# Kernel optimization log

Measured on AMD Instinct MI355X. Metric: run time of the kernel, lower is better.

Reference implementation:

```python
import jax, jax.numpy as jnp
import numpy as np
import math

EPS_NORM = 1e-6
EPS_COS = 1e-6


def _rms_norm(x, scale, eps):
    ms = jnp.mean(jnp.square(x), axis=-1, keepdims=True)
    return x * (scale * jax.lax.rsqrt(ms + eps))


def _apply_rope(x, theta):
    # x: [n, nh, s, e], theta: [n, nh, s, d] with 2*d <= e
    d = theta.shape[-1]
    x1, x2, rest = x[..., :d], x[..., d:2 * d], x[..., 2 * d:]
    cos, sin = jnp.cos(theta), jnp.sin(theta)
    y1 = x1 * cos - x2 * sin
    y2 = x2 * cos + x1 * sin
    return jnp.concatenate([y1, y2, rest], axis=-1)


def _make_freqs(d_head, n_heads):
    dim = d_head // 2
    log_min, log_max = math.log(math.pi), math.log(10.0 * math.pi)
    f = np.exp(np.linspace(log_min, log_max, n_heads * dim // 4 + 1, dtype=np.float64)[:-1])
    return jnp.asarray(f.reshape(dim // 4, n_heads).T, dtype=jnp.float32)  # [n_heads, dim//4]


def setup_inputs() -> dict:
    key = jax.random.key(0)
    ks = jax.random.split(key, 8)
    n, H, W, d_model = 4, 32, 32, 1024
    d_head, n_heads, cond_f = 64, 16, 1024
    x = jax.random.normal(ks[0], (n, H, W, d_model), dtype=jnp.float32)
    pos = jax.random.uniform(ks[1], (n, H, W, 2), dtype=jnp.float32) * 2.0 - 1.0
    cond = jax.random.normal(ks[2], (n, cond_f), dtype=jnp.float32)
    norm_scale = jnp.ones((d_model,), dtype=jnp.float32)
    ada_w = jax.random.normal(ks[3], (3 * d_model, cond_f), dtype=jnp.float32) * 0.02
    ada_b = jnp.zeros((3 * d_model,), dtype=jnp.float32)
    qkv_w = jax.random.normal(ks[4], (3 * d_model, d_model), dtype=jnp.float32) * 0.02
    attn_scale = jnp.full((n_heads,), 10.0, dtype=jnp.float32)
    out_w = jax.random.normal(ks[5], (d_model, d_model), dtype=jnp.float32) * 0.02
    freqs = _make_freqs(d_head, n_heads)
    return {"x": x, "pos": pos, "cond": cond, "norm_scale": norm_scale,
            "ada_w": ada_w, "ada_b": ada_b, "qkv_w": qkv_w,
            "attn_scale": attn_scale, "out_w": out_w, "freqs": freqs}


def reference(x, pos, cond, norm_scale, ada_w, ada_b, qkv_w, attn_scale, out_w, freqs):
    n, H, W, d_model = x.shape
    n_heads, nf = freqs.shape          # nf = d_head//4... actually (d_head//2)//4
    d_head = d_model // n_heads
    s = H * W
    skip = x
    # adaLN modulation
    mod = jax.nn.silu(cond) @ ada_w.T + ada_b              # [n, 3*d_model]
    shift, scale, gate = jnp.split(mod, 3, axis=-1)        # each [n, d_model]
    xn = _rms_norm(x, norm_scale, EPS_NORM)
    xm = xn * (1.0 + scale[:, None, None, :]) + shift[:, None, None, :]
    # qkv projection: layout (t nh e) on last dim
    qkv = (xm @ qkv_w.T).reshape(n, s, 3, n_heads, d_head)
    q, k, v = qkv[:, :, 0], qkv[:, :, 1], qkv[:, :, 2]     # [n, s, nh, e]
    q = jnp.transpose(q, (0, 2, 1, 3))                     # [n, nh, s, e]
    k = jnp.transpose(k, (0, 2, 1, 3))
    v = jnp.transpose(v, (0, 2, 1, 3))
    # cosine-sim scaling per head
    sqrt_scale = jnp.sqrt(attn_scale)[None, :, None, None]
    q = q * (sqrt_scale * jax.lax.rsqrt(jnp.sum(jnp.square(q), axis=-1, keepdims=True) + EPS_COS))
    k = k * (sqrt_scale * jax.lax.rsqrt(jnp.sum(jnp.square(k), axis=-1, keepdims=True) + EPS_COS))
    # axial RoPE angles
    posf = pos.reshape(n, s, 2)
    theta_h = posf[:, :, None, 0:1] * freqs                # [n, s, nh, nf]
    theta_w = posf[:, :, None, 1:2] * freqs
    theta = jnp.concatenate([theta_h, theta_w], axis=-1)   # [n, s, nh, 2*nf]
    theta = jnp.transpose(theta, (0, 2, 1, 3))             # [n, nh, s, 2*nf]
    q = _apply_rope(q, theta)
    k = _apply_rope(k, theta)
    # attention with softmax scale 1.0 (cosine-sim already scaled)
    scores = jnp.einsum('bnse,bnte->bnst', q, k)
    attn = jax.nn.softmax(scores, axis=-1)
    o = jnp.einsum('bnst,bnte->bnse', attn, v)             # [n, nh, s, e]
    o = jnp.transpose(o, (0, 2, 1, 3)).reshape(n, H, W, d_model)
    o = o @ out_w.T
    return skip + gate[:, None, None, :] * o
```

## Files before the change

### kernel.cpp

```cpp
#include <hip/hip_runtime.h>
#include <stdint.h>

typedef __bf16 bf16x8 __attribute__((ext_vector_type(8)));
typedef uint16_t u16x8 __attribute__((ext_vector_type(8)));
typedef uint16_t u16x4 __attribute__((ext_vector_type(4)));
typedef float f32x4 __attribute__((ext_vector_type(4)));

#define DEV static __device__ __forceinline__

DEV uint16_t f2bf(float f) {
  union { float f; uint32_t u; } v; v.f = f;
  return (uint16_t)((v.u + 0x8000u) >> 16);
}
DEV float bf2f(uint16_t h) {
  union { uint32_t u; float f; } v; v.u = ((uint32_t)h) << 16;
  return v.f;
}

#define GLOAD_LDS16(g, l)                                                     \
  __builtin_amdgcn_global_load_lds(                                           \
      (__attribute__((address_space(1))) void*)(g),                           \
      (__attribute__((address_space(3))) void*)(l), 16, 0, 0)

DEV void conv4(const float* __restrict__ src, uint16_t* __restrict__ dst, int n4,
               int tid, int nth) {
  const float4* s4 = (const float4*)src;
  for (int i = tid; i < n4; i += nth) {
    float4 v = s4[i];
    u16x4 o;
    o[0] = f2bf(v.x); o[1] = f2bf(v.y); o[2] = f2bf(v.z); o[3] = f2bf(v.w);
    *reinterpret_cast<u16x4*>(dst + (size_t)i * 4) = o;
  }
}

__global__ __launch_bounds__(256) void k_prep(
    const float* __restrict__ qkv_w, uint16_t* __restrict__ qkvw_bf,
    const float* __restrict__ out_w, uint16_t* __restrict__ outw_bf,
    const float* __restrict__ cond, const float* __restrict__ ada_w,
    const float* __restrict__ ada_b, float* __restrict__ mod) {
  int blk = blockIdx.x, t = threadIdx.x;
  if (blk < 3072) {
    int w = t >> 6, lane = t & 63;
    int gid = blk * 4 + w;
    int b = gid / 3072, j = gid - b * 3072;
    const float* cw = cond + b * 1024;
    const float* aw = ada_w + (size_t)j * 1024;
    float sum = 0.f;
    for (int i = 0; i < 16; ++i) {
      int f = lane + (i << 6);
      float c = cw[f];
      sum += (c / (1.f + __expf(-c))) * aw[f];
    }
    for (int m = 32; m; m >>= 1) sum += __shfl_xor(sum, m, 64);
    if (lane == 0) mod[b * 3072 + j] = sum + ada_b[j];
  } else if (blk < 3072 + 768) {
    conv4(qkv_w, qkvw_bf, 786432, (blk - 3072) * 256 + t, 768 * 256);
  } else {
    conv4(out_w, outw_bf, 262144, (blk - 3840) * 256 + t, 256 * 256);
  }
}

__global__ void k_norm_mod(const float* __restrict__ x, const float* __restrict__ norm_scale,
                           const float* __restrict__ mod, uint16_t* __restrict__ xm) {
  int row = blockIdx.x;
  int b = row >> 10;
  const float* xr = x + (size_t)row * 1024;
  const float* shiftp = mod + b * 3072;
  const float* scalep = shiftp + 1024;
  int t = threadIdx.x;
  float v[4];
  float s = 0.f;
  for (int i = 0; i < 4; ++i) { v[i] = xr[t + (i << 8)]; s += v[i] * v[i]; }
  for (int m = 32; m; m >>= 1) s += __shfl_xor(s, m, 64);
  __shared__ float red[4];
  if ((t & 63) == 0) red[t >> 6] = s;
  __syncthreads();
  s = red[0] + red[1] + red[2] + red[3];
  float inv = rsqrtf(s * (1.f / 1024.f) + 1e-6f);
  uint16_t* xo = xm + (size_t)row * 1024;
  for (int i = 0; i < 4; ++i) {
    int c = t + (i << 8);
    float val = v[i] * inv * norm_scale[c];
    val = val * (1.f + scalep[c]) + shiftp[c];
    xo[c] = f2bf(val);
  }
}

template <int N, int EPI>
__global__ __launch_bounds__(256) void k_gemm(const uint16_t* __restrict__ A,
                                              const uint16_t* __restrict__ B,
                                              uint16_t* __restrict__ Cbf,
                                              const float* __restrict__ skip,
                                              const float* __restrict__ modp,
                                              float* __restrict__ Cout) {
  constexpr int K = 1024;
  __shared__ uint16_t As[128 * 32];
  __shared__ uint16_t Bs[128 * 32];
  int t = threadIdx.x;
  int lane = t & 63;
  int w = t >> 6, wr = w >> 1, wc = w & 1;
  int bm = blockIdx.y, bn = blockIdx.x;
  f32x4 acc[4][4] = {};
  const size_t a_base = (size_t)(bm * 128) * K;
  const size_t b_base = (size_t)(bn * 128) * K;
  int r = t >> 2, cch = t & 3;
  for (int kt = 0; kt < K / 32; ++kt) {
    __syncthreads();
#pragma unroll
    for (int i = 0; i < 2; ++i) {
      int rr = r + (i << 6);
      int cs = (cch ^ ((rr >> 1) & 3)) << 3;
      GLOAD_LDS16(A + a_base + (size_t)rr * K + kt * 32 + cs, As + rr * 32 + (cch << 3));
      GLOAD_LDS16(B + b_base + (size_t)rr * K + kt * 32 + cs, Bs + rr * 32 + (cch << 3));
    }
    __syncthreads();
    bf16x8 af[4], bfr[4];
    int lq = lane >> 4;
#pragma unroll
    for (int m = 0; m < 4; ++m) {
      int R = wr * 64 + m * 16 + (lane & 15);
      af[m] = *reinterpret_cast<const bf16x8*>(&As[R * 32 + ((lq ^ ((R >> 1) & 3)) << 3)]);
    }
#pragma unroll
    for (int n = 0; n < 4; ++n) {
      int R = wc * 64 + n * 16 + (lane & 15);
      bfr[n] = *reinterpret_cast<const bf16x8*>(&Bs[R * 32 + ((lq ^ ((R >> 1) & 3)) << 3)]);
    }
#pragma unroll
    for (int m = 0; m < 4; ++m)
#pragma unroll
      for (int n = 0; n < 4; ++n)
        acc[m][n] = __builtin_amdgcn_mfma_f32_16x16x32_bf16(af[m], bfr[n], acc[m][n], 0, 0, 0);
  }
  int row0 = bm * 128 + wr * 64;
  int col0 = bn * 128 + wc * 64;
#pragma unroll
  for (int m = 0; m < 4; ++m)
#pragma unroll
    for (int n = 0; n < 4; ++n)
#pragma unroll
      for (int rr = 0; rr < 4; ++rr) {
        int R = row0 + m * 16 + ((lane >> 4) << 2) + rr;
        int C = col0 + n * 16 + (lane & 15);
        float v = acc[m][n][rr];
        if (EPI == 0) {
          Cbf[(size_t)R * N + C] = f2bf(v);
        } else {
          float g = modp[(R >> 10) * 3072 + 2048 + C];
          Cout[(size_t)R * N + C] = skip[(size_t)R * N + C] + g * v;
        }
      }
}

__global__ __launch_bounds__(256) void k_qkvpost(
    const uint16_t* __restrict__ qkv, const float* __restrict__ pos,
    const float* __restrict__ freqs, const float* __restrict__ attn_scale,
    uint16_t* __restrict__ Qb, uint16_t* __restrict__ Kb, uint16_t* __restrict__ Vt) {
  __shared__ uint16_t vtile[64 * 66];
  int t = threadIdx.x;
  int st = blockIdx.x, bh = blockIdx.y;
  int b = bh >> 4, h = bh & 15;
  int r = t >> 2;
  int s = t & 3;
  int sp = st * 64 + r;
  size_t m = (size_t)b * 1024 + sp;
  const uint16_t* basep = qkv + m * 3072 + h * 64 + s * 16;
  bf16x8 q0 = *reinterpret_cast<const bf16x8*>(basep);
  bf16x8 q1 = *reinterpret_cast<const bf16x8*>(basep + 8);
  bf16x8 k0 = *reinterpret_cast<const bf16x8*>(basep + 1024);
  bf16x8 k1 = *reinterpret_cast<const bf16x8*>(basep + 1032);
  u16x8 v0 = *reinterpret_cast<const u16x8*>(basep + 2048);
  u16x8 v1 = *reinterpret_cast<const u16x8*>(basep + 2056);
  float qv[16], kv[16];
#pragma unroll
  for (int i = 0; i < 8; ++i) {
    qv[i] = (float)q0[i]; qv[8 + i] = (float)q1[i];
    kv[i] = (float)k0[i]; kv[8 + i] = (float)k1[i];
  }
  float sq = 0.f, sk = 0.f;
#pragma unroll
  for (int i = 0; i < 16; ++i) { sq += qv[i] * qv[i]; sk += kv[i] * kv[i]; }
  sq += __shfl_xor(sq, 1, 64); sq += __shfl_xor(sq, 2, 64);
  sk += __shfl_xor(sk, 1, 64); sk += __shfl_xor(sk, 2, 64);
  float ss = sqrtf(attn_scale[h]);
  float qs = ss * rsqrtf(sq + 1e-6f);
  float ks = ss * rsqrtf(sk + 1e-6f);
#pragma unroll
  for (int i = 0; i < 16; ++i) { qv[i] *= qs; kv[i] *= ks; }
  float p0 = pos[m * 2], p1 = pos[m * 2 + 1];
  float sgn = (s == 0) ? -1.f : 1.f;
#pragma unroll
  for (int i = 0; i < 16; ++i) {
    float pq = __shfl_xor(qv[i], 1, 64);
    float pk = __shfl_xor(kv[i], 1, 64);
    if (s < 2) {
      float th = ((i < 8) ? p0 : p1) * freqs[h * 8 + (i & 7)];
      float sn, cs;
      __sincosf(th, &sn, &cs);
      qv[i] = qv[i] * cs + sgn * pq * sn;
      kv[i] = kv[i] * cs + sgn * pk * sn;
    }
  }
  bf16x8 qo0, qo1, ko0, ko1;
#pragma unroll
  for (int i = 0; i < 8; ++i) {
    qo0[i] = (__bf16)qv[i]; qo1[i] = (__bf16)qv[8 + i];
    ko0[i] = (__bf16)kv[i]; ko1[i] = (__bf16)kv[8 + i];
  }
  size_t qkb = ((size_t)bh * 1024 + sp) * 64 + s * 16;
  *reinterpret_cast<bf16x8*>(Qb + qkb) = qo0;
  *reinterpret_cast<bf16x8*>(Qb + qkb + 8) = qo1;
  *reinterpret_cast<bf16x8*>(Kb + qkb) = ko0;
  *reinterpret_cast<bf16x8*>(Kb + qkb + 8) = ko1;
#pragma unroll
  for (int i = 0; i < 8; ++i) {
    vtile[(s * 16 + i) * 66 + r] = v0[i];
    vtile[(s * 16 + 8 + i) * 66 + r] = v1[i];
  }
  __syncthreads();
  int d = t >> 2, c = t & 3;
  u16x8 w0, w1;
#pragma unroll
  for (int i = 0; i < 8; ++i) {
    w0[i] = vtile[d * 66 + c * 16 + i];
    w1[i] = vtile[d * 66 + c * 16 + 8 + i];
  }
  size_t vb = ((size_t)bh * 64 + d) * 1024 + st * 64 + c * 16;
  *reinterpret_cast<u16x8*>(Vt + vb) = w0;
  *reinterpret_cast<u16x8*>(Vt + vb + 8) = w1;
}

__global__ __launch_bounds__(512) void k_attn(const uint16_t* __restrict__ Qb,
                                              const uint16_t* __restrict__ Kb,
                                              const uint16_t* __restrict__ Vt,
                                              uint16_t* __restrict__ obuf) {
  __shared__ uint16_t Ks[64 * 64];
  __shared__ uint16_t Vs[64 * 64];
  __shared__ uint16_t Ps[8][16 * 88];
  int t = threadIdx.x, lane = t & 63, w = t >> 6;
  int qt = blockIdx.y, bh = blockIdx.x;
  int b = bh >> 4, h = bh & 15;
  int qrow = qt * 128 + w * 16 + (lane & 15);
  int klo = (lane >> 4) << 3;
  const uint16_t* qptr = Qb + ((size_t)bh * 1024 + qrow) * 64 + klo;
  bf16x8 qf0 = *reinterpret_cast<const bf16x8*>(qptr);
  bf16x8 qf1 = *reinterpret_cast<const bf16x8*>(qptr + 32);
  f32x4 oacc[4] = {};
  float denom[4] = {0.f, 0.f, 0.f, 0.f};
  const size_t kbase = (size_t)bh * 1024 * 64;
  const size_t vbase = (size_t)bh * 64 * 1024;
  for (int kt = 0; kt < 16; ++kt) {
    __syncthreads();
    {
      int row = t >> 3;
      int ce = ((t & 7) ^ (row & 7)) << 3;
      GLOAD_LDS16(Kb + kbase + (size_t)(kt * 64 + row) * 64 + ce, Ks + t * 8);
      GLOAD_LDS16(Vt + vbase + (size_t)row * 1024 + kt * 64 + ce, Vs + t * 8);
    }
    __syncthreads();
    bf16x8 pa0, pa1;
    {
      f32x4 s[4];
      for (int n = 0; n < 4; ++n) {
        int row = n * 16 + (lane & 15);
        int sw = (row & 7) << 3;
        bf16x8 kf0 = *reinterpret_cast<const bf16x8*>(&Ks[row * 64 + (klo ^ sw)]);
        bf16x8 kf1 = *reinterpret_cast<const bf16x8*>(&Ks[row * 64 + ((32 + klo) ^ sw)]);
        f32x4 z = {};
        z = __builtin_amdgcn_mfma_f32_16x16x32_bf16(qf0, kf0, z, 0, 0, 0);
        z = __builtin_amdgcn_mfma_f32_16x16x32_bf16(qf1, kf1, z, 0, 0, 0);
        s[n] = z;
      }
      for (int n = 0; n < 4; ++n)
        for (int rr = 0; rr < 4; ++rr) {
          float p = __expf(s[n][rr]);
          denom[rr] += p;
          Ps[w][(((lane >> 4) << 2) + rr) * 88 + n * 16 + (lane & 15)] = f2bf(p);
        }
      pa0 = *reinterpret_cast<const bf16x8*>(&Ps[w][(lane & 15) * 88 + klo]);
      pa1 = *reinterpret_cast<const bf16x8*>(&Ps[w][(lane & 15) * 88 + 32 + klo]);
    }
    for (int dt = 0; dt < 4; ++dt) {
      int row = dt * 16 + (lane & 15);
      int sw = (row & 7) << 3;
      bf16x8 vf0 = *reinterpret_cast<const bf16x8*>(&Vs[row * 64 + (klo ^ sw)]);
      bf16x8 vf1 = *reinterpret_cast<const bf16x8*>(&Vs[row * 64 + ((32 + klo) ^ sw)]);
      oacc[dt] = __builtin_amdgcn_mfma_f32_16x16x32_bf16(pa0, vf0, oacc[dt], 0, 0, 0);
      oacc[dt] = __builtin_amdgcn_mfma_f32_16x16x32_bf16(pa1, vf1, oacc[dt], 0, 0, 0);
    }
  }
  for (int rr = 0; rr < 4; ++rr)
    for (int msk = 8; msk; msk >>= 1) denom[rr] += __shfl_xor(denom[rr], msk, 64);
  for (int rr = 0; rr < 4; ++rr) {
    float rinv = 1.f / denom[rr];
    int sp = qt * 128 + w * 16 + ((lane >> 4) << 2) + rr;
    size_t orow = ((size_t)b * 1024 + sp) * 1024 + h * 64;
    for (int dt = 0; dt < 4; ++dt)
      obuf[orow + dt * 16 + (lane & 15)] = f2bf(oacc[dt][rr] * rinv);
  }
}

extern "C" void kernel_launch(void* const* d_in, const int* in_sizes, int n_in,
                              void* d_out, int out_size, void* d_ws, size_t ws_size,
                              hipStream_t stream) {
  const float* x = (const float*)d_in[0];
  const float* pos = (const float*)d_in[1];
  const float* cond = (const float*)d_in[2];
  const float* norm_scale = (const float*)d_in[3];
  const float* ada_w = (const float*)d_in[4];
  const float* ada_b = (const float*)d_in[5];
  const float* qkv_w = (const float*)d_in[6];
  const float* attn_scale = (const float*)d_in[7];
  const float* out_w = (const float*)d_in[8];
  const float* freqs = (const float*)d_in[9];
  float* out = (float*)d_out;
  char* ws = (char*)d_ws;
  float* mod = (float*)(ws + 0);
  uint16_t* xm = (uint16_t*)(ws + 65536);
  uint16_t* qkvw_bf = (uint16_t*)(ws + 8454144);
  uint16_t* outw_bf = (uint16_t*)(ws + 14745600);
  uint16_t* qkv = (uint16_t*)(ws + 16842752);
  uint16_t* Qb = (uint16_t*)(ws + 42008576);
  uint16_t* Kb = (uint16_t*)(ws + 50397184);
  uint16_t* Vt = (uint16_t*)(ws + 58785792);
  uint16_t* obuf = (uint16_t*)(ws + 67174400);

  k_prep<<<dim3(4096), dim3(256), 0, stream>>>(qkv_w, qkvw_bf, out_w, outw_bf,
                                               cond, ada_w, ada_b, mod);
  k_norm_mod<<<dim3(4096), dim3(256), 0, stream>>>(x, norm_scale, mod, xm);
  k_gemm<3072, 0><<<dim3(24, 32), dim3(256), 0, stream>>>(xm, qkvw_bf, qkv, nullptr, nullptr, nullptr);
  k_qkvpost<<<dim3(16, 64), dim3(256), 0, stream>>>(qkv, pos, freqs, attn_scale, Qb, Kb, Vt);
  k_attn<<<dim3(64, 8), dim3(512), 0, stream>>>(Qb, Kb, Vt, obuf);
  k_gemm<1024, 1><<<dim3(8, 32), dim3(256), 0, stream>>>(obuf, outw_bf, nullptr, x, mod, out);
}
```

Baseline: 118.2 us.

## Vectorize norm kernel, shrink out-proj GEMM tile, fold log2e into Q scaling

The RMS-norm/modulation kernel now reads float4 vectors and writes four bf16 values per thread instead of strided scalar accesses. The output projection GEMM gets its own kernel with 128x64 tiles, launching 512 blocks instead of 256 so more CUs are busy on the 1024-wide output. The log2(e) factor is folded into the Q scale so attention can use exp2f in place of __expf. The smaller tile lowers data reuse per block, and the exp2 rewrite is only mathematically equivalent up to rounding.

```diff
diff --git a/kernel.cpp b/kernel.cpp
--- a/kernel.cpp
+++ b/kernel.cpp
@@ -11,10 +11,6 @@
 DEV uint16_t f2bf(float f) {
   union { float f; uint32_t u; } v; v.f = f;
   return (uint16_t)((v.u + 0x8000u) >> 16);
-}
-DEV float bf2f(uint16_t h) {
-  union { uint32_t u; float f; } v; v.u = ((uint32_t)h) << 16;
-  return v.f;
 }
 
 #define GLOAD_LDS16(g, l)                                                     \
@@ -64,36 +60,33 @@
                            const float* __restrict__ mod, uint16_t* __restrict__ xm) {
   int row = blockIdx.x;
   int b = row >> 10;
-  const float* xr = x + (size_t)row * 1024;
-  const float* shiftp = mod + b * 3072;
-  const float* scalep = shiftp + 1024;
   int t = threadIdx.x;
-  float v[4];
-  float s = 0.f;
-  for (int i = 0; i < 4; ++i) { v[i] = xr[t + (i << 8)]; s += v[i] * v[i]; }
+  const float4* xr4 = (const float4*)(x + (size_t)row * 1024);
+  const float4* ns4 = (const float4*)norm_scale;
+  const float4* sh4 = (const float4*)(mod + b * 3072);
+  const float4* sc4 = (const float4*)(mod + b * 3072 + 1024);
+  float4 v = xr4[t];
+  float s = v.x * v.x + v.y * v.y + v.z * v.z + v.w * v.w;
   for (int m = 32; m; m >>= 1) s += __shfl_xor(s, m, 64);
   __shared__ float red[4];
   if ((t & 63) == 0) red[t >> 6] = s;
   __syncthreads();
   s = red[0] + red[1] + red[2] + red[3];
   float inv = rsqrtf(s * (1.f / 1024.f) + 1e-6f);
-  uint16_t* xo = xm + (size_t)row * 1024;
-  for (int i = 0; i < 4; ++i) {
-    int c = t + (i << 8);
-    float val = v[i] * inv * norm_scale[c];
-    val = val * (1.f + scalep[c]) + shiftp[c];
-    xo[c] = f2bf(val);
-  }
-}
-
-template <int N, int EPI>
-__global__ __launch_bounds__(256) void k_gemm(const uint16_t* __restrict__ A,
-                                              const uint16_t* __restrict__ B,
-                                              uint16_t* __restrict__ Cbf,
-                                              const float* __restrict__ skip,
-                                              const float* __restrict__ modp,
-                                              float* __restrict__ Cout) {
+  float4 ns = ns4[t], sh = sh4[t], sc = sc4[t];
+  u16x4 o;
+  o[0] = f2bf(v.x * inv * ns.x * (1.f + sc.x) + sh.x);
+  o[1] = f2bf(v.y * inv * ns.y * (1.f + sc.y) + sh.y);
+  o[2] = f2bf(v.z * inv * ns.z * (1.f + sc.z) + sh.z);
+  o[3] = f2bf(v.w * inv * ns.w * (1.f + sc.w) + sh.w);
+  *reinterpret_cast<u16x4*>(xm + (size_t)row * 1024 + t * 4) = o;
+}
+
+__global__ __launch_bounds__(256) void k_gemmqkv(const uint16_t* __restrict__ A,
+                                                 const uint16_t* __restrict__ B,
+                                                 uint16_t* __restrict__ Cbf) {
   constexpr int K = 1024;
+  constexpr int N = 3072;
   __shared__ uint16_t As[128 * 32];
   __shared__ uint16_t Bs[128 * 32];
   int t = threadIdx.x;
@@ -142,13 +135,71 @@
       for (int rr = 0; rr < 4; ++rr) {
         int R = row0 + m * 16 + ((lane >> 4) << 2) + rr;
         int C = col0 + n * 16 + (lane & 15);
-        float v = acc[m][n][rr];
-        if (EPI == 0) {
-          Cbf[(size_t)R * N + C] = f2bf(v);
-        } else {
-          float g = modp[(R >> 10) * 3072 + 2048 + C];
-          Cout[(size_t)R * N + C] = skip[(size_t)R * N + C] + g * v;
-        }
+        Cbf[(size_t)R * N + C] = f2bf(acc[m][n][rr]);
+      }
+}
+
+__global__ __launch_bounds__(256) void k_gemmout(const uint16_t* __restrict__ A,
+                                                 const uint16_t* __restrict__ B,
+                                                 const float* __restrict__ skip,
+                                                 const float* __restrict__ modp,
+                                                 float* __restrict__ Cout) {
+  constexpr int K = 1024;
+  constexpr int N = 1024;
+  __shared__ uint16_t As[128 * 32];
+  __shared__ uint16_t Bs[64 * 32];
+  int t = threadIdx.x;
+  int lane = t & 63;
+  int w = t >> 6;
+  int bm = blockIdx.y, bn = blockIdx.x;
+  f32x4 acc[2][4] = {};
+  const size_t a_base = (size_t)(bm * 128) * K;
+  const size_t b_base = (size_t)(bn * 64) * K;
+  int r = t >> 2, cch = t & 3;
+  for (int kt = 0; kt < K / 32; ++kt) {
+    __syncthreads();
+#pragma unroll
+    for (int i = 0; i < 2; ++i) {
+      int rr = r + (i << 6);
+      int cs = (cch ^ ((rr >> 1) & 3)) << 3;
+      GLOAD_LDS16(A + a_base + (size_t)rr * K + kt * 32 + cs, As + rr * 32 + (cch << 3));
+    }
+    {
+      int rr = r;
+      int cs = (cch ^ ((rr >> 1) & 3)) << 3;
+      GLOAD_LDS16(B + b_base + (size_t)rr * K + kt * 32 + cs, Bs + rr * 32 + (cch << 3));
+    }
+    __syncthreads();
+    bf16x8 af[2], bfr[4];
+    int lq = lane >> 4;
+#pragma unroll
+    for (int m = 0; m < 2; ++m) {
+      int R = w * 32 + m * 16 + (lane & 15);
+      af[m] = *reinterpret_cast<const bf16x8*>(&As[R * 32 + ((lq ^ ((R >> 1) & 3)) << 3)]);
+    }
+#pragma unroll
+    for (int n = 0; n < 4; ++n) {
+      int R = n * 16 + (lane & 15);
+      bfr[n] = *reinterpret_cast<const bf16x8*>(&Bs[R * 32 + ((lq ^ ((R >> 1) & 3)) << 3)]);
+    }
+#pragma unroll
+    for (int m = 0; m < 2; ++m)
+#pragma unroll
+      for (int n = 0; n < 4; ++n)
+        acc[m][n] = __builtin_amdgcn_mfma_f32_16x16x32_bf16(af[m], bfr[n], acc[m][n], 0, 0, 0);
+  }
+  int row0 = bm * 128 + w * 32;
+  int col0 = bn * 64;
+#pragma unroll
+  for (int m = 0; m < 2; ++m)
+#pragma unroll
+    for (int n = 0; n < 4; ++n)
+#pragma unroll
+      for (int rr = 0; rr < 4; ++rr) {
+        int R = row0 + m * 16 + ((lane >> 4) << 2) + rr;
+        int C = col0 + n * 16 + (lane & 15);
+        float g = modp[(R >> 10) * 3072 + 2048 + C];
+        Cout[(size_t)R * N + C] = skip[(size_t)R * N + C] + g * acc[m][n][rr];
       }
 }
 
@@ -183,7 +234,7 @@
   sq += __shfl_xor(sq, 1, 64); sq += __shfl_xor(sq, 2, 64);
   sk += __shfl_xor(sk, 1, 64); sk += __shfl_xor(sk, 2, 64);
   float ss = sqrtf(attn_scale[h]);
-  float qs = ss * rsqrtf(sq + 1e-6f);
+  float qs = ss * 1.4426950408889634f * rsqrtf(sq + 1e-6f);
   float ks = ss * rsqrtf(sk + 1e-6f);
 #pragma unroll
   for (int i = 0; i < 16; ++i) { qv[i] *= qs; kv[i] *= ks; }
@@ -273,7 +324,7 @@
       }
       for (int n = 0; n < 4; ++n)
         for (int rr = 0; rr < 4; ++rr) {
-          float p = __expf(s[n][rr]);
+          float p = exp2f(s[n][rr]);
           denom[rr] += p;
           Ps[w][(((lane >> 4) << 2) + rr) * 88 + n * 16 + (lane & 15)] = f2bf(p);
         }
@@ -328,8 +379,8 @@
   k_prep<<<dim3(4096), dim3(256), 0, stream>>>(qkv_w, qkvw_bf, out_w, outw_bf,
                                                cond, ada_w, ada_b, mod);
   k_norm_mod<<<dim3(4096), dim3(256), 0, stream>>>(x, norm_scale, mod, xm);
-  k_gemm<3072, 0><<<dim3(24, 32), dim3(256), 0, stream>>>(xm, qkvw_bf, qkv, nullptr, nullptr, nullptr);
+  k_gemmqkv<<<dim3(24, 32), dim3(256), 0, stream>>>(xm, qkvw_bf, qkv);
   k_qkvpost<<<dim3(16, 64), dim3(256), 0, stream>>>(qkv, pos, freqs, attn_scale, Qb, Kb, Vt);
   k_attn<<<dim3(64, 8), dim3(512), 0, stream>>>(Qb, Kb, Vt, obuf);
-  k_gemm<1024, 1><<<dim3(8, 32), dim3(256), 0, stream>>>(obuf, outw_bf, nullptr, x, mod, out);
-}
+  k_gemmout<<<dim3(16, 32), dim3(256), 0, stream>>>(obuf, outw_bf, x, mod, out);
+}
```

Result: no change. 118.7 us (+0.4%).
